# Kernel optimization log

Measured on AMD Instinct MI355X. Metric: run time of the kernel, lower is better.

The kernel has to match this reference:

```python
import jax, jax.numpy as jnp
import numpy as np

B, S, D, H = 2, 4096, 1024, 16
DK = D // H


def setup_inputs() -> dict:
    key = jax.random.key(0)
    ks = jax.random.split(key, 8)
    scale = 1.0 / np.sqrt(D)
    return {
        "q": jax.random.normal(ks[0], (B, S, D), dtype=jnp.float32),
        "k": jax.random.normal(ks[1], (B, S, D), dtype=jnp.float32),
        "v": jax.random.normal(ks[2], (B, S, D), dtype=jnp.float32),
        "mask": jax.random.randint(ks[3], (1, 1, S, S), 0, 2, dtype=jnp.int32),
        "w_q": jax.random.normal(ks[4], (D, D), dtype=jnp.float32) * scale,
        "w_k": jax.random.normal(ks[5], (D, D), dtype=jnp.float32) * scale,
        "w_v": jax.random.normal(ks[6], (D, D), dtype=jnp.float32) * scale,
        "w_o": jax.random.normal(ks[7], (D, D), dtype=jnp.float32) * scale,
    }


def reference(q, k, v, mask, w_q, w_k, w_v, w_o):
    # torch Linear(bias=False): y = x @ W.T
    def proj_split(x, w):
        y = jnp.einsum("bsd,ed->bse", x, w)  # [B,S,D]
        return y.reshape(x.shape[0], -1, H, DK).transpose(0, 2, 1, 3)  # [B,H,S,dk]

    Q = proj_split(q, w_q)
    K = proj_split(k, w_k)
    V = proj_split(v, w_v)

    scores = jnp.einsum("bhqd,bhkd->bhqk", Q, K) / jnp.sqrt(jnp.float32(DK))
    scores = jnp.where(mask == 0, jnp.float32(-1e9), scores)
    attn = jax.nn.softmax(scores, axis=-1)  # dropout p=0 -> identity
    ctx = jnp.einsum("bhqk,bhkd->bhqd", attn, V)  # [B,H,S,dk]
    ctx = ctx.transpose(0, 2, 1, 3).reshape(q.shape[0], -1, D)  # [B,S,D]
    return jnp.einsum("bsd,ed->bse", ctx, w_o)
```

## Files before the change

### kernel.cpp

```cpp
#include <hip/hip_runtime.h>
#include <math.h>
#include <stdint.h>

constexpr int B = 2, S = 4096, D = 1024, H = 16, DK = 64;
constexpr int M_TOT = B * S;

typedef __attribute__((ext_vector_type(8))) short bf16x8;
typedef __attribute__((ext_vector_type(4))) float f32x4;
typedef __attribute__((ext_vector_type(4))) uint32_t u32x4;
typedef unsigned short u16;

__device__ inline u16 f2bf(float f) {
    uint32_t u = __builtin_bit_cast(uint32_t, f);
    u += 0x7fffu + ((u >> 16) & 1u);
    return (u16)(u >> 16);
}

__device__ inline u16 f2bf_hw(float f) {
    __bf16 h = (__bf16)f;
    return __builtin_bit_cast(u16, h);
}

__device__ inline void gl2lds16(const void* g, void* l) {
    __builtin_amdgcn_global_load_lds((const __attribute__((address_space(1))) void*)g,
                                     (__attribute__((address_space(3))) void*)l, 16, 0, 0);
}

__global__ __launch_bounds__(256) void conv_bf16(const float* __restrict__ s0, const float* __restrict__ s1,
                                                 const float* __restrict__ s2, const float* __restrict__ s3,
                                                 u16* __restrict__ d0, u16* __restrict__ d1,
                                                 u16* __restrict__ d2, u16* __restrict__ d3, int n) {
    const float* s; u16* d;
    switch (blockIdx.y) {
        case 0: s = s0; d = d0; break;
        case 1: s = s1; d = d1; break;
        case 2: s = s2; d = d2; break;
        default: s = s3; d = d3; break;
    }
    const int i = (blockIdx.x * 256 + threadIdx.x) * 4;
    if (i < n) {
        float4 v = *(const float4*)(s + i);
        ushort4 o;
        o.x = f2bf(v.x); o.y = f2bf(v.y); o.z = f2bf(v.z); o.w = f2bf(v.w);
        *(ushort4*)(d + i) = o;
    }
}

__global__ __launch_bounds__(256) void mask_pack(const int* __restrict__ m, uint32_t* __restrict__ out) {
    const int i = blockIdx.x * 256 + threadIdx.x;
    const int base = i * 32;
    uint32_t b = 0;
#pragma unroll
    for (int j = 0; j < 32; ++j) b |= (m[base + j] != 0 ? 1u : 0u) << j;
    out[i] = b;
}

template <typename OutT>
__global__ __launch_bounds__(256) void gemm_bt(const u16* __restrict__ X, const u16* __restrict__ Wm,
                                               OutT* __restrict__ Y, int M, int N, int K, float oscale) {
    __shared__ u16 As[128 * 64];
    __shared__ u16 Bs[128 * 64];
    const int tid = threadIdx.x;
    const int lane = tid & 63;
    const int wave = tid >> 6;
    const int l15 = lane & 15;
    const int quad = lane >> 4;
    const int i0 = blockIdx.x * 128;
    const int j0 = blockIdx.y * 128;
    const int wm = wave & 1, wn = wave >> 1;
    const int lr = lane >> 3;
    const int lc = (lane & 7) * 8;

    f32x4 zero = {0.f, 0.f, 0.f, 0.f};
    f32x4 acc[4][4];
#pragma unroll
    for (int a = 0; a < 4; ++a)
#pragma unroll
        for (int b2 = 0; b2 < 4; ++b2) acc[a][b2] = zero;

    for (int k0 = 0; k0 < K; k0 += 64) {
#pragma unroll
        for (int c = 0; c < 4; ++c) {
            const int ch = wave * 4 + c;
            const int row = ch * 8 + lr;
            gl2lds16(X + (size_t)(i0 + row) * K + k0 + lc, &As[ch * 512]);
            gl2lds16(Wm + (size_t)(j0 + row) * K + k0 + lc, &Bs[ch * 512]);
        }
        __syncthreads();
        bf16x8 af[4][2];
#pragma unroll
        for (int mt = 0; mt < 4; ++mt)
#pragma unroll
            for (int ks = 0; ks < 2; ++ks)
                af[mt][ks] = *(const bf16x8*)&As[(wm * 64 + mt * 16 + l15) * 64 + ks * 32 + quad * 8];
#pragma unroll
        for (int nt = 0; nt < 4; ++nt) {
#pragma unroll
            for (int ks = 0; ks < 2; ++ks) {
                bf16x8 bfr = *(const bf16x8*)&Bs[(wn * 64 + nt * 16 + l15) * 64 + ks * 32 + quad * 8];
#pragma unroll
                for (int mt = 0; mt < 4; ++mt)
                    acc[mt][nt] = __builtin_amdgcn_mfma_f32_16x16x32_bf16(af[mt][ks], bfr, acc[mt][nt], 0, 0, 0);
            }
        }
        __syncthreads();
    }
#pragma unroll
    for (int mt = 0; mt < 4; ++mt) {
#pragma unroll
        for (int r = 0; r < 4; ++r) {
            const int gi = i0 + wm * 64 + mt * 16 + quad * 4 + r;
#pragma unroll
            for (int nt = 0; nt < 4; ++nt) {
                const int gj = j0 + wn * 64 + nt * 16 + l15;
                const float v = acc[mt][nt][r] * oscale;
                if constexpr (sizeof(OutT) == 2) {
                    Y[(size_t)gi * N + gj] = (OutT)f2bf(v);
                } else {
                    Y[(size_t)gi * N + gj] = v;
                }
            }
        }
    }
}

struct KVStage {
    bf16x8 rk[2];
    uint64_t rva[2], rvb[2];
    uint64_t rm[2];
};

__global__ __launch_bounds__(256) void attn_mfma(const u16* __restrict__ Qb, const u16* __restrict__ Kb,
                                                 const u16* __restrict__ Vt,
                                                 const uint64_t* __restrict__ mask64,
                                                 u16* __restrict__ ctx) {
    __shared__ u16 Ks[64 * 64];
    __shared__ u16 Vs[64 * 64];
    const int tid = threadIdx.x;
    const int lane = tid & 63;
    const int wave = tid >> 6;
    const int l15 = lane & 15;
    const int quad = lane >> 4;

    const int bid = blockIdx.y * (S / 128) + blockIdx.x;
    const int xcd = bid & 7;
    const int loc = bid >> 3;
    const int bh = xcd * 4 + (loc >> 5);
    const int q0 = (loc & 31) * 128;

    const int bb = bh >> 4, hh = bh & 15;
    const int mbase = bb * S;
    const int e0 = hh * DK;
    const int r7 = l15 & 7;

    const int srow = tid >> 2;
    const int scb = tid & 3;

    bf16x8 aq[2][2];
#pragma unroll
    for (int mi = 0; mi < 2; ++mi) {
        const u16* qrow = Qb + (size_t)(mbase + q0 + wave * 32 + mi * 16 + l15) * D + e0;
        aq[mi][0] = *(const bf16x8*)(qrow + quad * 8);
        aq[mi][1] = *(const bf16x8*)(qrow + 32 + quad * 8);
    }

    f32x4 O[2][4];
    f32x4 Ol[2];
#pragma unroll
    for (int mi = 0; mi < 2; ++mi) {
        Ol[mi] = (f32x4){0.f, 0.f, 0.f, 0.f};
#pragma unroll
        for (int dt = 0; dt < 4; ++dt) O[mi][dt] = (f32x4){0.f, 0.f, 0.f, 0.f};
    }

    bf16x8 ONES;
#pragma unroll
    for (int i = 0; i < 8; ++i) ONES[i] = (short)0x3F80;

    const uint64_t* mrow[2];
#pragma unroll
    for (int mi = 0; mi < 2; ++mi)
        mrow[mi] = mask64 + (size_t)(q0 + wave * 32 + mi * 16 + l15) * (S / 64);

    auto LOADT = [&](KVStage& st, int kt) {
        const int kb = kt * 64;
#pragma unroll
        for (int it = 0; it < 2; ++it) {
            const int cb = scb + it * 4;
            st.rk[it] = *(const bf16x8*)(Kb + (size_t)(mbase + kb + srow) * D + e0 + cb * 8);
            const int k0v = 32 * (cb >> 2) + 4 * (cb & 3);
            const u16* vsrc = Vt + (size_t)(e0 + srow) * M_TOT + mbase + kb + k0v;
            st.rva[it] = *(const uint64_t*)(vsrc);
            st.rvb[it] = *(const uint64_t*)(vsrc + 16);
        }
#pragma unroll
        for (int mi = 0; mi < 2; ++mi) st.rm[mi] = mrow[mi][kt];
    };

    auto WRITET = [&](const KVStage& st) {
#pragma unroll
        for (int it = 0; it < 2; ++it) {
            const int cb = scb + it * 4;
            const int phys = cb ^ (srow & 7);
            *(bf16x8*)&Ks[srow * 64 + phys * 8] = st.rk[it];
            *(uint64_t*)&Vs[srow * 64 + phys * 8] = st.rva[it];
            *(uint64_t*)&Vs[srow * 64 + phys * 8 + 4] = st.rvb[it];
        }
    };

    auto COMPUTE = [&](const KVStage& st) {
        bf16x8 kf[4][2];
#pragma unroll
        for (int nt = 0; nt < 4; ++nt) {
            kf[nt][0] = *(const bf16x8*)&Ks[(nt * 16 + l15) * 64 + (quad ^ r7) * 8];
            kf[nt][1] = *(const bf16x8*)&Ks[(nt * 16 + l15) * 64 + ((quad + 4) ^ r7) * 8];
        }

        bf16x8 ap[2][2];
#pragma unroll
        for (int mi = 0; mi < 2; ++mi) {
            f32x4 sa[4];
            __builtin_amdgcn_s_setprio(1);
#pragma unroll
            for (int nt = 0; nt < 4; ++nt) {
                f32x4 c = {0.f, 0.f, 0.f, 0.f};
                c = __builtin_amdgcn_mfma_f32_16x16x32_bf16(kf[nt][0], aq[mi][0], c, 0, 0, 0);
                c = __builtin_amdgcn_mfma_f32_16x16x32_bf16(kf[nt][1], aq[mi][1], c, 0, 0, 0);
                sa[nt] = c;
            }
            __builtin_amdgcn_s_setprio(0);
            const uint64_t mw = st.rm[mi];
            const uint32_t mlo = (uint32_t)(mw >> (quad * 4));
            const uint32_t mhi = (uint32_t)(mw >> (quad * 4 + 32));
            uint32_t pk[4][2];
#pragma unroll
            for (int nt = 0; nt < 4; ++nt) {
                const uint32_t mx = (nt < 2) ? mlo : mhi;
                float p[4];
#pragma unroll
                for (int r = 0; r < 4; ++r) {
                    const float e = __builtin_amdgcn_exp2f(sa[nt][r]);
                    p[r] = ((mx >> ((nt & 1) * 16 + r)) & 1u) ? e : 0.f;
                }
                pk[nt][0] = (uint32_t)f2bf_hw(p[0]) | ((uint32_t)f2bf_hw(p[1]) << 16);
                pk[nt][1] = (uint32_t)f2bf_hw(p[2]) | ((uint32_t)f2bf_hw(p[3]) << 16);
            }
            const u32x4 w0 = {pk[0][0], pk[0][1], pk[1][0], pk[1][1]};
            const u32x4 w1 = {pk[2][0], pk[2][1], pk[3][0], pk[3][1]};
            ap[mi][0] = __builtin_bit_cast(bf16x8, w0);
            ap[mi][1] = __builtin_bit_cast(bf16x8, w1);
        }

        __builtin_amdgcn_s_setprio(1);
#pragma unroll
        for (int mi = 0; mi < 2; ++mi) {
            Ol[mi] = __builtin_amdgcn_mfma_f32_16x16x32_bf16(ap[mi][0], ONES, Ol[mi], 0, 0, 0);
            Ol[mi] = __builtin_amdgcn_mfma_f32_16x16x32_bf16(ap[mi][1], ONES, Ol[mi], 0, 0, 0);
        }
#pragma unroll
        for (int dt = 0; dt < 4; ++dt) {
            const bf16x8 bv0 = *(const bf16x8*)&Vs[(dt * 16 + l15) * 64 + (quad ^ r7) * 8];
            const bf16x8 bv1 = *(const bf16x8*)&Vs[(dt * 16 + l15) * 64 + ((quad + 4) ^ r7) * 8];
#pragma unroll
            for (int mi = 0; mi < 2; ++mi) {
                O[mi][dt] = __builtin_amdgcn_mfma_f32_16x16x32_bf16(ap[mi][0], bv0, O[mi][dt], 0, 0, 0);
                O[mi][dt] = __builtin_amdgcn_mfma_f32_16x16x32_bf16(ap[mi][1], bv1, O[mi][dt], 0, 0, 0);
            }
        }
        __builtin_amdgcn_s_setprio(0);
    };

    KVStage stA, stB;
    LOADT(stA, 0);
    for (int kt = 0; kt < S / 64; kt += 2) {
        LOADT(stB, kt + 1);
        __builtin_amdgcn_s_barrier();
        WRITET(stA);
        asm volatile("s_waitcnt lgkmcnt(0)" ::: "memory");
        __builtin_amdgcn_s_barrier();
        __builtin_amdgcn_sched_barrier(0);
        COMPUTE(stA);

        if (kt + 2 < S / 64) LOADT(stA, kt + 2);
        __builtin_amdgcn_s_barrier();
        WRITET(stB);
        asm volatile("s_waitcnt lgkmcnt(0)" ::: "memory");
        __builtin_amdgcn_s_barrier();
        __builtin_amdgcn_sched_barrier(0);
        COMPUTE(stB);
    }

#pragma unroll
    for (int mi = 0; mi < 2; ++mi) {
#pragma unroll
        for (int r = 0; r < 4; ++r) {
            const float inv = 1.f / Ol[mi][r];
            const int gm = mbase + q0 + wave * 32 + mi * 16 + quad * 4 + r;
#pragma unroll
            for (int dt = 0; dt < 4; ++dt)
                ctx[(size_t)gm * D + e0 + dt * 16 + l15] = f2bf(O[mi][dt][r] * inv);
        }
    }
}

extern "C" void kernel_launch(void* const* d_in, const int* in_sizes, int n_in,
                              void* d_out, int out_size, void* d_ws, size_t ws_size,
                              hipStream_t stream) {
    (void)in_sizes; (void)n_in; (void)out_size; (void)ws_size;
    const float* q = (const float*)d_in[0];
    const float* k = (const float*)d_in[1];
    const float* v = (const float*)d_in[2];
    const int* msk = (const int*)d_in[3];
    const float* w_q = (const float*)d_in[4];
    const float* w_k = (const float*)d_in[5];
    const float* w_v = (const float*)d_in[6];
    const float* w_o = (const float*)d_in[7];
    float* out = (float*)d_out;

    const size_t MB = 1u << 20;
    char* w = (char*)d_ws;
    u16* qb   = (u16*)(w + 0 * MB);
    u16* kb   = (u16*)(w + 16 * MB);
    u16* vb   = (u16*)(w + 32 * MB);
    u16* wqb  = (u16*)(w + 48 * MB);
    u16* wkb  = (u16*)(w + 50 * MB);
    u16* wvb  = (u16*)(w + 52 * MB);
    u16* wob  = (u16*)(w + 54 * MB);
    uint64_t* maskb = (uint64_t*)(w + 56 * MB);
    u16* Qf   = (u16*)(w + 58 * MB);
    u16* Kf   = (u16*)(w + 74 * MB);
    u16* Vtf  = (u16*)(w + 90 * MB);
    u16* ctxb = (u16*)(w + 106 * MB);

    const float SCL2 = 0.18033688011112042f;

    dim3 blk(256);
    conv_bf16<<<dim3(8192, 3), blk, 0, stream>>>(q, k, v, q, qb, kb, vb, qb, M_TOT * D);
    conv_bf16<<<dim3(1024, 4), blk, 0, stream>>>(w_q, w_k, w_v, w_o, wqb, wkb, wvb, wob, D * D);
    mask_pack<<<dim3(S * S / 32 / 256), blk, 0, stream>>>(msk, (uint32_t*)maskb);

    gemm_bt<u16><<<dim3(M_TOT / 128, D / 128), blk, 0, stream>>>(qb, wqb, Qf, M_TOT, D, D, SCL2);
    gemm_bt<u16><<<dim3(M_TOT / 128, D / 128), blk, 0, stream>>>(kb, wkb, Kf, M_TOT, D, D, 1.0f);
    gemm_bt<u16><<<dim3(D / 128, M_TOT / 128), blk, 0, stream>>>(wvb, vb, Vtf, D, M_TOT, D, 1.0f);

    attn_mfma<<<dim3(S / 128, B * H), blk, 0, stream>>>(Qf, Kf, Vtf, maskb, ctxb);

    gemm_bt<float><<<dim3(M_TOT / 128, D / 128), blk, 0, stream>>>(ctxb, wob, out, M_TOT, D, D, 1.0f);
}
```

Baseline: 516.1 us.

## Double-buffer GEMM LDS tiles and rework attention K/V LDS swizzle

```diff
diff --git a/kernel.cpp b/kernel.cpp
--- a/kernel.cpp
+++ b/kernel.cpp
@@ -58,8 +58,8 @@
 template <typename OutT>
 __global__ __launch_bounds__(256) void gemm_bt(const u16* __restrict__ X, const u16* __restrict__ Wm,
                                                OutT* __restrict__ Y, int M, int N, int K, float oscale) {
-    __shared__ u16 As[128 * 64];
-    __shared__ u16 Bs[128 * 64];
+    __shared__ u16 As[2][128 * 64];
+    __shared__ u16 Bs[2][128 * 64];
     const int tid = threadIdx.x;
     const int lane = tid & 63;
     const int wave = tid >> 6;
@@ -78,33 +78,55 @@
 #pragma unroll
         for (int b2 = 0; b2 < 4; ++b2) acc[a][b2] = zero;
 
-    for (int k0 = 0; k0 < K; k0 += 64) {
+    auto STAGE = [&](int buf, int k0) {
 #pragma unroll
         for (int c = 0; c < 4; ++c) {
             const int ch = wave * 4 + c;
             const int row = ch * 8 + lr;
-            gl2lds16(X + (size_t)(i0 + row) * K + k0 + lc, &As[ch * 512]);
-            gl2lds16(Wm + (size_t)(j0 + row) * K + k0 + lc, &Bs[ch * 512]);
-        }
-        __syncthreads();
+            gl2lds16(X + (size_t)(i0 + row) * K + k0 + lc, &As[buf][ch * 512]);
+            gl2lds16(Wm + (size_t)(j0 + row) * K + k0 + lc, &Bs[buf][ch * 512]);
+        }
+    };
+
+    auto COMPUTE = [&](int buf) {
         bf16x8 af[4][2];
 #pragma unroll
         for (int mt = 0; mt < 4; ++mt)
 #pragma unroll
             for (int ks = 0; ks < 2; ++ks)
-                af[mt][ks] = *(const bf16x8*)&As[(wm * 64 + mt * 16 + l15) * 64 + ks * 32 + quad * 8];
+                af[mt][ks] = *(const bf16x8*)&As[buf][(wm * 64 + mt * 16 + l15) * 64 + ks * 32 + quad * 8];
 #pragma unroll
         for (int nt = 0; nt < 4; ++nt) {
 #pragma unroll
             for (int ks = 0; ks < 2; ++ks) {
-                bf16x8 bfr = *(const bf16x8*)&Bs[(wn * 64 + nt * 16 + l15) * 64 + ks * 32 + quad * 8];
+                bf16x8 bfr = *(const bf16x8*)&Bs[buf][(wn * 64 + nt * 16 + l15) * 64 + ks * 32 + quad * 8];
 #pragma unroll
                 for (int mt = 0; mt < 4; ++mt)
                     acc[mt][nt] = __builtin_amdgcn_mfma_f32_16x16x32_bf16(af[mt][ks], bfr, acc[mt][nt], 0, 0, 0);
             }
         }
-        __syncthreads();
-    }
+    };
+
+    const int KT = K >> 6;
+    STAGE(0, 0);
+    asm volatile("s_waitcnt vmcnt(0)" ::: "memory");
+    __builtin_amdgcn_s_barrier();
+    __builtin_amdgcn_sched_barrier(0);
+    for (int t = 0; t < KT; t += 2) {
+        if (t + 1 < KT) STAGE(1, (t + 1) << 6);
+        COMPUTE(0);
+        asm volatile("s_waitcnt vmcnt(0)" ::: "memory");
+        __builtin_amdgcn_s_barrier();
+        __builtin_amdgcn_sched_barrier(0);
+        if (t + 2 < KT) STAGE(0, (t + 2) << 6);
+        if (t + 1 < KT) {
+            COMPUTE(1);
+            asm volatile("s_waitcnt vmcnt(0)" ::: "memory");
+            __builtin_amdgcn_s_barrier();
+            __builtin_amdgcn_sched_barrier(0);
+        }
+    }
+
 #pragma unroll
     for (int mt = 0; mt < 4; ++mt) {
 #pragma unroll
@@ -151,10 +173,11 @@
     const int bb = bh >> 4, hh = bh & 15;
     const int mbase = bb * S;
     const int e0 = hh * DK;
-    const int r7 = l15 & 7;
+    const int swr = ((l15 & 3) << 1) | ((l15 >> 2) & 1);
 
     const int srow = tid >> 2;
     const int scb = tid & 3;
+    const int sws = ((srow & 3) << 1) | ((srow >> 2) & 1);
 
     bf16x8 aq[2][2];
 #pragma unroll
@@ -201,10 +224,11 @@
 #pragma unroll
         for (int it = 0; it < 2; ++it) {
             const int cb = scb + it * 4;
-            const int phys = cb ^ (srow & 7);
+            const int phys = cb ^ sws;
             *(bf16x8*)&Ks[srow * 64 + phys * 8] = st.rk[it];
-            *(uint64_t*)&Vs[srow * 64 + phys * 8] = st.rva[it];
-            *(uint64_t*)&Vs[srow * 64 + phys * 8 + 4] = st.rvb[it];
+            const u32x4 vv = {(uint32_t)st.rva[it], (uint32_t)(st.rva[it] >> 32),
+                              (uint32_t)st.rvb[it], (uint32_t)(st.rvb[it] >> 32)};
+            *(u32x4*)&Vs[srow * 64 + phys * 8] = vv;
         }
     };
 
@@ -212,8 +236,8 @@
         bf16x8 kf[4][2];
 #pragma unroll
         for (int nt = 0; nt < 4; ++nt) {
-            kf[nt][0] = *(const bf16x8*)&Ks[(nt * 16 + l15) * 64 + (quad ^ r7) * 8];
-            kf[nt][1] = *(const bf16x8*)&Ks[(nt * 16 + l15) * 64 + ((quad + 4) ^ r7) * 8];
+            kf[nt][0] = *(const bf16x8*)&Ks[(nt * 16 + l15) * 64 + (quad ^ swr) * 8];
+            kf[nt][1] = *(const bf16x8*)&Ks[(nt * 16 + l15) * 64 + ((quad + 4) ^ swr) * 8];
         }
 
         bf16x8 ap[2][2];
@@ -259,8 +283,8 @@
         }
 #pragma unroll
         for (int dt = 0; dt < 4; ++dt) {
-            const bf16x8 bv0 = *(const bf16x8*)&Vs[(dt * 16 + l15) * 64 + (quad ^ r7) * 8];
-            const bf16x8 bv1 = *(const bf16x8*)&Vs[(dt * 16 + l15) * 64 + ((quad + 4) ^ r7) * 8];
+            const bf16x8 bv0 = *(const bf16x8*)&Vs[(dt * 16 + l15) * 64 + (quad ^ swr) * 8];
+            const bf16x8 bv1 = *(const bf16x8*)&Vs[(dt * 16 + l15) * 64 + ((quad + 4) ^ swr) * 8];
 #pragma unroll
             for (int mi = 0; mi < 2; ++mi) {
                 O[mi][dt] = __builtin_amdgcn_mfma_f32_16x16x32_bf16(ap[mi][0], bv0, O[mi][dt], 0, 0, 0);
```

Measured after the change: 518.1 us. No clear change (+0.4%).
